# Kernel tuning notes

Measured on AMD Instinct MI355X. Metric: run time of the kernel, lower is better.

## Reference

```python
import jax, jax.numpy as jnp
import numpy as np

N = 100_000   # number of sparse points
C = 128       # channels
K3 = 27       # 3x3x3 kernel offsets


def sparse_conv(x, nbr, W, b):
    """Minkowski-style sparse conv: gather-GEMM-scatter.
    x:   [N, Cin] point features
    nbr: [N, K3] neighbor index per kernel offset; index N -> missing (zero row)
    W:   [K3, Cin, Cout], b: [Cout]
    """
    x_pad = jnp.concatenate([x, jnp.zeros((1, x.shape[1]), x.dtype)], axis=0)

    def step(acc, wk_nk):
        Wk, nk = wk_nk                      # Wk: [Cin,Cout], nk: [N]
        return acc + x_pad[nk] @ Wk, None   # gather + GEMM, accumulate

    acc0 = jnp.broadcast_to(b, (x.shape[0], W.shape[2])).astype(x.dtype)
    acc, _ = jax.lax.scan(step, acc0, (W, nbr.T))
    return acc


def setup_inputs() -> dict:
    key = jax.random.key(0)
    ks = jax.random.split(key, 12)
    Ch = C // 2

    def w(k, shape, fan_in):
        return jax.random.normal(k, shape, dtype=jnp.float32) / np.sqrt(fan_in)

    x = jax.random.normal(ks[0], (N, C), dtype=jnp.float32)
    # neighbor map; value N means "no neighbor" (maps to zero-padded row)
    nbr = jax.random.randint(ks[1], (N, K3), 0, N + 1, dtype=jnp.int32)

    return {
        "x": x,
        "nbr": nbr,
        "W00": w(ks[2], (K3, C, Ch), K3 * C),   # conv0_0: kxkxk, C -> C/2
        "b00": jnp.zeros((Ch,), jnp.float32),
        "W01": w(ks[3], (K3, Ch, Ch), K3 * Ch),  # conv0_1: kxkxk, C/2 -> C/2
        "b01": jnp.zeros((Ch,), jnp.float32),
        "W10": w(ks[4], (C, Ch), C),             # conv1_0: 1x1x1, C -> C/2
        "b10": jnp.zeros((Ch,), jnp.float32),
        "W11": w(ks[5], (K3, Ch, Ch), K3 * Ch),  # conv1_1: kxkxk, C/2 -> C/2
        "b11": jnp.zeros((Ch,), jnp.float32),
        "W12": w(ks[6], (Ch, Ch), Ch),           # conv1_2: 1x1x1, C/2 -> C/2
        "b12": jnp.zeros((Ch,), jnp.float32),
    }


def reference(x, nbr, W00, b00, W01, b01, W10, b10, W11, b11, W12, b12):
    # branch 0: conv -> relu -> conv
    h0 = jax.nn.relu(sparse_conv(x, nbr, W00, b00))
    out0 = sparse_conv(h0, nbr, W01, b01)
    # branch 1: 1x1 conv -> relu -> conv -> relu -> 1x1 conv
    h1 = jax.nn.relu(x @ W10 + b10)
    h1 = jax.nn.relu(sparse_conv(h1, nbr, W11, b11))
    out1 = h1 @ W12 + b12
    # concat channels, residual add
    return jnp.concatenate([out0, out1], axis=1) + x
```

## Files before the change

### kernel.cpp

```cpp
#include <hip/hip_runtime.h>
#include <hip/hip_bf16.h>
#include <stdint.h>

typedef __bf16 bf16x8 __attribute__((ext_vector_type(8)));
typedef float  f32x4  __attribute__((ext_vector_type(4)));

#define MFMA(A, B, C) __builtin_amdgcn_mfma_f32_16x16x32_bf16((A), (B), (C), 0, 0, 0)

#define LDS_BARRIER() asm volatile("s_waitcnt lgkmcnt(0)\n\ts_barrier" ::: "memory")

static __device__ __forceinline__ unsigned short f2b(float f) {
    union { float f; unsigned int u; } v; v.f = f;
    return (unsigned short)((v.u + 0x7FFFu + ((v.u >> 16) & 1u)) >> 16);
}

__global__ __launch_bounds__(256) void convert_kernel(
    const float* __restrict__ x, unsigned short* __restrict__ xb,
    unsigned short* __restrict__ hb, int N) {
    long long i = (long long)blockIdx.x * blockDim.x + threadIdx.x;
    long long base = i * 4;
    long long nx = (long long)N * 128;
    long long total = nx + 128;
    if (base >= total) return;
    if (base < nx) {
        float4 v = *(const float4*)(x + base);
        ushort4 o;
        o.x = f2b(v.x); o.y = f2b(v.y); o.z = f2b(v.z); o.w = f2b(v.w);
        *(ushort4*)(xb + base) = o;
    } else {
        ushort4 z = make_ushort4(0, 0, 0, 0);
        *(ushort4*)(xb + base) = z;
        *(ushort4*)(hb + base) = z;
    }
}

__global__ __launch_bounds__(256) void pack_kernel(
    const float* __restrict__ W00, const float* __restrict__ W01,
    const float* __restrict__ W10, const float* __restrict__ W11,
    const float* __restrict__ W12,
    unsigned short* __restrict__ wp00, unsigned short* __restrict__ wpC,
    unsigned short* __restrict__ wp10, unsigned short* __restrict__ wp12) {
    int g = blockIdx.x * blockDim.x + threadIdx.x;
    const float* W; int cinSteps; int which;
    if (g < 27648)      { W = W00; cinSteps = 4; which = 0; }
    else if (g < 41472) { g -= 27648; W = W01; cinSteps = 2; which = 1; }
    else if (g < 55296) { g -= 41472; W = W11; cinSteps = 2; which = 2; }
    else if (g < 56320) { g -= 55296; W = W10; cinSteps = 4; which = 3; }
    else if (g < 56832) { g -= 56320; W = W12; cinSteps = 2; which = 4; }
    else return;
    int lane = g & 63;
    int st   = g >> 6;
    int t    = st & 3;
    int s    = st >> 2;
    int q = lane >> 4, n16 = lane & 15;
    int k    = s / cinSteps;
    int cinb = (s % cinSteps) * 32;
    int Cin  = cinSteps * 32;
    int cout = t * 16 + n16;
    unsigned short o[8];
#pragma unroll
    for (int j = 0; j < 8; ++j) {
        float v = W[(size_t)(k * Cin + cinb + q * 8 + j) * 64 + cout];
        o[j] = f2b(v);
    }
    unsigned short* dst;
    if (which == 0)      dst = wp00 + (size_t)g * 8;
    else if (which == 1) dst = wpC + (size_t)k * 8192 +
                               ((size_t)(((s & 1) * 4 + t) * 64 + lane)) * 8;
    else if (which == 2) dst = wpC + (size_t)k * 8192 + 4096 +
                               ((size_t)(((s & 1) * 4 + t) * 64 + lane)) * 8;
    else if (which == 3) dst = wp10 + (size_t)g * 8;
    else                 dst = wp12 + (size_t)g * 8;
    *(ushort4*)(dst)     = make_ushort4(o[0], o[1], o[2], o[3]);
    *(ushort4*)(dst + 4) = make_ushort4(o[4], o[5], o[6], o[7]);
}

__global__ __launch_bounds__(256, 2) void passB_kernel(
    const unsigned short* __restrict__ xb, const int* __restrict__ nbr,
    const unsigned short* __restrict__ wp00, const unsigned short* __restrict__ wp10,
    const float* __restrict__ b00, const float* __restrict__ b10,
    unsigned short* __restrict__ hb, int N) {
    __shared__ __align__(16) unsigned short bbuf[2][8192];
    __shared__ __align__(16) int lds_idx[256 * 27];
    const int tid  = threadIdx.x;
    const int lane = tid & 63;
    const int wv   = tid >> 6;
    const int q = lane >> 4, n16 = lane & 15;
    const int rowbase = blockIdx.x * 256 + wv * 64;

    int4 br[4];
#pragma unroll
    for (int j = 0; j < 4; ++j) br[j] = *(const int4*)(wp00 + j * 2048 + tid * 8);
    {
        long long gbase = (long long)blockIdx.x * 256 * 27;
        long long lim = (long long)N * 27 - 1;
        for (int i = tid; i < 6912; i += 256) {
            long long gi = gbase + i; if (gi > lim) gi = lim;
            lds_idx[i] = nbr[gi];
        }
    }
#pragma unroll
    for (int j = 0; j < 4; ++j) *(int4*)(&bbuf[0][j * 2048 + tid * 8]) = br[j];
    __syncthreads();

    f32x4 acc0[4][4];
    f32x4 acc1[4][4];
#pragma unroll
    for (int rs = 0; rs < 4; ++rs)
#pragma unroll
        for (int t = 0; t < 4; ++t) { acc0[rs][t] = (f32x4)0.f; acc1[rs][t] = (f32x4)0.f; }

    int idxb[4], own[4];
#pragma unroll
    for (int rs = 0; rs < 4; ++rs) {
        idxb[rs] = (wv * 64 + rs * 16 + n16) * 27;
        own[rs]  = min(rowbase + rs * 16 + n16, N - 1);
    }

    bf16x8 D[4][4];
#pragma unroll
    for (int rs = 0; rs < 4; ++rs) {
        const unsigned short* p = xb + (size_t)lds_idx[idxb[rs]] * 128 + q * 8;
#pragma unroll
        for (int s2 = 0; s2 < 4; ++s2) D[rs][s2] = *(const bf16x8*)(p + s2 * 32);
    }

    for (int k = 0; k < 27; ++k) {
        int buf = k & 1;
        if (k < 26) {
            const unsigned short* src = wp00 + (size_t)(k + 1) * 8192;
#pragma unroll
            for (int j = 0; j < 4; ++j) br[j] = *(const int4*)(src + j * 2048 + tid * 8);
        }
        bf16x8 Dn[4][4];
#pragma unroll
        for (int rs = 0; rs < 4; ++rs) {
            int ian = (k + 1 < 27) ? lds_idx[idxb[rs] + k + 1] : own[rs];
            const unsigned short* p = xb + (size_t)ian * 128 + q * 8;
#pragma unroll
            for (int s2 = 0; s2 < 4; ++s2) Dn[rs][s2] = *(const bf16x8*)(p + s2 * 32);
        }
        const unsigned short* lb = &bbuf[buf][0];
#pragma unroll
        for (int s2 = 0; s2 < 4; ++s2) {
#pragma unroll
            for (int t = 0; t < 4; ++t) {
                bf16x8 B = *(const bf16x8*)(lb + (s2 * 4 + t) * 512 + lane * 8);
#pragma unroll
                for (int rs = 0; rs < 4; ++rs)
                    acc0[rs][t] = MFMA(D[rs][s2], B, acc0[rs][t]);
            }
        }
        if (k < 26) {
#pragma unroll
            for (int j = 0; j < 4; ++j)
                *(int4*)(&bbuf[buf ^ 1][j * 2048 + tid * 8]) = br[j];
        }
#pragma unroll
        for (int rs = 0; rs < 4; ++rs)
#pragma unroll
            for (int s2 = 0; s2 < 4; ++s2) D[rs][s2] = Dn[rs][s2];
        LDS_BARRIER();
    }

#pragma unroll
    for (int s2 = 0; s2 < 4; ++s2) {
#pragma unroll
        for (int t = 0; t < 4; ++t) {
            bf16x8 B = *(const bf16x8*)(wp10 + s2 * 2048 + t * 512 + lane * 8);
#pragma unroll
            for (int rs = 0; rs < 4; ++rs)
                acc1[rs][t] = MFMA(D[rs][s2], B, acc1[rs][t]);
        }
    }

#pragma unroll
    for (int rs = 0; rs < 4; ++rs)
#pragma unroll
        for (int t = 0; t < 4; ++t) {
            int col = t * 16 + n16;
            float bb0 = b00[col], bb1 = b10[col];
#pragma unroll
            for (int r = 0; r < 4; ++r) {
                int row = rowbase + rs * 16 + q * 4 + r;
                if (row < N) {
                    hb[(size_t)row * 128 + col]      = f2b(fmaxf(acc0[rs][t][r] + bb0, 0.f));
                    hb[(size_t)row * 128 + 64 + col] = f2b(fmaxf(acc1[rs][t][r] + bb1, 0.f));
                }
            }
        }
}

__global__ __launch_bounds__(256, 3) void passC_kernel(
    const unsigned short* __restrict__ hb, const int* __restrict__ nbr,
    const float* __restrict__ x,
    const unsigned short* __restrict__ wpC, const unsigned short* __restrict__ wp12,
    const float* __restrict__ b01, const float* __restrict__ b11,
    const float* __restrict__ b12, float* __restrict__ out, int N) {
    __shared__ __align__(16) unsigned short bbuf[2][4096];
    __shared__ __align__(16) int lds_idx[128 * 27];
    const int tid  = threadIdx.x;
    const int lane = tid & 63;
    const int wv   = tid >> 6;
    const int q = lane >> 4, n16 = lane & 15;
    const int rowbase = blockIdx.x * 128 + wv * 32;

    int idxb[2];
#pragma unroll
    for (int rs = 0; rs < 2; ++rs) idxb[rs] = (wv * 32 + rs * 16 + n16) * 27;

    {
        int4 br[2];
#pragma unroll
        for (int j = 0; j < 2; ++j) br[j] = *(const int4*)(wpC + j * 2048 + tid * 8);
        {
            long long gbase = (long long)blockIdx.x * 128 * 27;
            long long lim = (long long)N * 27 - 1;
            for (int i = tid; i < 3456; i += 256) {
                long long gi = gbase + i; if (gi > lim) gi = lim;
                lds_idx[i] = nbr[gi];
            }
        }
#pragma unroll
        for (int j = 0; j < 2; ++j) *(int4*)(&bbuf[0][j * 2048 + tid * 8]) = br[j];
        __syncthreads();

        f32x4 accA[2][4];
#pragma unroll
        for (int rs = 0; rs < 2; ++rs)
#pragma unroll
            for (int t = 0; t < 4; ++t) accA[rs][t] = (f32x4)0.f;

        bf16x8 Da[2][2], Db[2][2], Dc[2][2];
#pragma unroll
        for (int rs = 0; rs < 2; ++rs) {
            const unsigned short* p0 = hb + (size_t)lds_idx[idxb[rs] + 0] * 128 + q * 8;
            Da[rs][0] = *(const bf16x8*)(p0);
            Da[rs][1] = *(const bf16x8*)(p0 + 32);
            const unsigned short* p1 = hb + (size_t)lds_idx[idxb[rs] + 1] * 128 + q * 8;
            Db[rs][0] = *(const bf16x8*)(p1);
            Db[rs][1] = *(const bf16x8*)(p1 + 32);
        }

        for (int k = 0; k < 27; ++k) {
            int buf = k & 1;
            if (k < 26) {
                const unsigned short* src = wpC + (size_t)(k + 1) * 8192;
#pragma unroll
                for (int j = 0; j < 2; ++j)
                    br[j] = *(const int4*)(src + j * 2048 + tid * 8);
            }
#pragma unroll
            for (int rs = 0; rs < 2; ++rs) {
                int j2 = min(k + 2, 26);
                const unsigned short* p =
                    hb + (size_t)lds_idx[idxb[rs] + j2] * 128 + q * 8;
                Dc[rs][0] = *(const bf16x8*)(p);
                Dc[rs][1] = *(const bf16x8*)(p + 32);
            }
            const unsigned short* lb = &bbuf[buf][0];
#pragma unroll
            for (int s2 = 0; s2 < 2; ++s2) {
#pragma unroll
                for (int t = 0; t < 4; ++t) {
                    bf16x8 B = *(const bf16x8*)(lb + (s2 * 4 + t) * 512 + lane * 8);
#pragma unroll
                    for (int rs = 0; rs < 2; ++rs)
                        accA[rs][t] = MFMA(Da[rs][s2], B, accA[rs][t]);
                }
            }
            if (k < 26) {
#pragma unroll
                for (int j = 0; j < 2; ++j)
                    *(int4*)(&bbuf[buf ^ 1][j * 2048 + tid * 8]) = br[j];
            }
#pragma unroll
            for (int rs = 0; rs < 2; ++rs)
#pragma unroll
                for (int s2 = 0; s2 < 2; ++s2) {
                    Da[rs][s2] = Db[rs][s2]; Db[rs][s2] = Dc[rs][s2];
                }
            LDS_BARRIER();
        }

#pragma unroll
        for (int rs = 0; rs < 2; ++rs)
#pragma unroll
            for (int t = 0; t < 4; ++t) {
                int col = t * 16 + n16;
                float bo = b01[col];
#pragma unroll
                for (int r = 0; r < 4; ++r) {
                    int row = rowbase + rs * 16 + q * 4 + r;
                    if (row < N) {
                        float xv = __builtin_nontemporal_load(x + (size_t)row * 128 + col);
                        __builtin_nontemporal_store(accA[rs][t][r] + bo + xv,
                                                    out + (size_t)row * 128 + col);
                    }
                }
            }
    }

    {
        int4 br[2];
#pragma unroll
        for (int j = 0; j < 2; ++j)
            br[j] = *(const int4*)(wpC + 4096 + j * 2048 + tid * 8);
#pragma unroll
        for (int j = 0; j < 2; ++j) *(int4*)(&bbuf[0][j * 2048 + tid * 8]) = br[j];
        __syncthreads();

        f32x4 accT[2][4];
#pragma unroll
        for (int rs = 0; rs < 2; ++rs)
#pragma unroll
            for (int t = 0; t < 4; ++t) accT[rs][t] = (f32x4)0.f;

        bf16x8 Da[2][2], Db[2][2], Dc[2][2];
#pragma unroll
        for (int rs = 0; rs < 2; ++rs) {
            const unsigned short* p0 =
                hb + (size_t)lds_idx[idxb[rs] + 0] * 128 + 64 + q * 8;
            Da[rs][0] = *(const bf16x8*)(p0);
            Da[rs][1] = *(const bf16x8*)(p0 + 32);
            const unsigned short* p1 =
                hb + (size_t)lds_idx[idxb[rs] + 1] * 128 + 64 + q * 8;
            Db[rs][0] = *(const bf16x8*)(p1);
            Db[rs][1] = *(const bf16x8*)(p1 + 32);
        }

        for (int k = 0; k < 27; ++k) {
            int buf = k & 1;
            if (k < 26) {
                const unsigned short* src = wpC + 4096 + (size_t)(k + 1) * 8192;
#pragma unroll
                for (int j = 0; j < 2; ++j)
                    br[j] = *(const int4*)(src + j * 2048 + tid * 8);
            }
#pragma unroll
            for (int rs = 0; rs < 2; ++rs) {
                int j2 = min(k + 2, 26);
                const unsigned short* p =
                    hb + (size_t)lds_idx[idxb[rs] + j2] * 128 + 64 + q * 8;
                Dc[rs][0] = *(const bf16x8*)(p);
                Dc[rs][1] = *(const bf16x8*)(p + 32);
            }
            const unsigned short* lb = &bbuf[buf][0];
#pragma unroll
            for (int s2 = 0; s2 < 2; ++s2) {
#pragma unroll
                for (int t = 0; t < 4; ++t) {
                    bf16x8 B = *(const bf16x8*)(lb + (s2 * 4 + t) * 512 + lane * 8);
#pragma unroll
                    for (int rs = 0; rs < 2; ++rs)
                        accT[rs][t] = MFMA(Da[rs][s2], B, accT[rs][t]);
                }
            }
            if (k < 26) {
#pragma unroll
                for (int j = 0; j < 2; ++j)
                    *(int4*)(&bbuf[buf ^ 1][j * 2048 + tid * 8]) = br[j];
            }
#pragma unroll
            for (int rs = 0; rs < 2; ++rs)
#pragma unroll
                for (int s2 = 0; s2 < 2; ++s2) {
                    Da[rs][s2] = Db[rs][s2]; Db[rs][s2] = Dc[rs][s2];
                }
            LDS_BARRIER();
        }

        unsigned short* myl = (wv < 3) ? ((unsigned short*)lds_idx + wv * 2304)
                                       : &bbuf[0][0];
#pragma unroll
        for (int rs = 0; rs < 2; ++rs)
#pragma unroll
            for (int t = 0; t < 4; ++t) {
                int col = t * 16 + n16;
                float bt = b11[col];
#pragma unroll
                for (int r = 0; r < 4; ++r) {
                    float tv = fmaxf(accT[rs][t][r] + bt, 0.f);
                    myl[(rs * 16 + q * 4 + r) * 72 + col] = f2b(tv);
                }
            }

        f32x4 accO1[2][4];
#pragma unroll
        for (int rs = 0; rs < 2; ++rs)
#pragma unroll
            for (int t = 0; t < 4; ++t) accO1[rs][t] = (f32x4)0.f;
#pragma unroll
        for (int s2 = 0; s2 < 2; ++s2) {
#pragma unroll
            for (int t = 0; t < 4; ++t) {
                bf16x8 B = *(const bf16x8*)(wp12 + s2 * 2048 + t * 512 + lane * 8);
#pragma unroll
                for (int rs = 0; rs < 2; ++rs) {
                    bf16x8 A = *(const bf16x8*)(myl + (rs * 16 + n16) * 72 + s2 * 32 + q * 8);
                    accO1[rs][t] = MFMA(A, B, accO1[rs][t]);
                }
            }
        }
#pragma unroll
        for (int rs = 0; rs < 2; ++rs)
#pragma unroll
            for (int t = 0; t < 4; ++t) {
                int col = t * 16 + n16;
                float bo = b12[col];
#pragma unroll
                for (int r = 0; r < 4; ++r) {
                    int row = rowbase + rs * 16 + q * 4 + r;
                    if (row < N) {
                        float xv = __builtin_nontemporal_load(x + (size_t)row * 128 + 64 + col);
                        __builtin_nontemporal_store(accO1[rs][t][r] + bo + xv,
                                                    out + (size_t)row * 128 + 64 + col);
                    }
                }
            }
    }
}

extern "C" void kernel_launch(void* const* d_in, const int* in_sizes, int n_in,
                              void* d_out, int out_size, void* d_ws, size_t ws_size,
                              hipStream_t stream) {
    const float* x   = (const float*)d_in[0];
    const int*   nbr = (const int*)d_in[1];
    const float* W00 = (const float*)d_in[2];
    const float* b00 = (const float*)d_in[3];
    const float* W01 = (const float*)d_in[4];
    const float* b01 = (const float*)d_in[5];
    const float* W10 = (const float*)d_in[6];
    const float* b10 = (const float*)d_in[7];
    const float* W11 = (const float*)d_in[8];
    const float* b11 = (const float*)d_in[9];
    const float* W12 = (const float*)d_in[10];
    const float* b12 = (const float*)d_in[11];
    float* out = (float*)d_out;
    int N = in_sizes[0] / 128;

    char* ws = (char*)d_ws;
    size_t cur = 0;
    unsigned short* xb  = (unsigned short*)(ws + cur); cur += (size_t)(N + 1) * 128 * 2;
    unsigned short* hb  = (unsigned short*)(ws + cur); cur += (size_t)(N + 1) * 128 * 2;
    unsigned short* wp00 = (unsigned short*)(ws + cur); cur += 27648 * 8 * 2;
    unsigned short* wpC  = (unsigned short*)(ws + cur); cur += (size_t)27 * 8192 * 2;
    unsigned short* wp10 = (unsigned short*)(ws + cur); cur += 8192 * 2;
    unsigned short* wp12 = (unsigned short*)(ws + cur); cur += 4096 * 2;

    long long cvt_groups = ((long long)N * 128 + 128) / 4;
    int cvt_blocks = (int)((cvt_groups + 255) / 256);
    convert_kernel<<<cvt_blocks, 256, 0, stream>>>(x, xb, hb, N);
    pack_kernel<<<222, 256, 0, stream>>>(W00, W01, W10, W11, W12,
                                         wp00, wpC, wp10, wp12);
    int nstripsB = (N + 255) / 256;
    passB_kernel<<<nstripsB, 256, 0, stream>>>(xb, nbr, wp00, wp10, b00, b10, hb, N);
    int nstripsC = (N + 127) / 128;
    passC_kernel<<<nstripsC, 256, 0, stream>>>(hb, nbr, x, wpC, wp12,
                                               b01, b11, b12, out, N);
}
```

Baseline: 393.1 us.

## Split passB input channels into two phases and merge prep kernels

The first sparse conv is restructured into two passes over the 128 input channels, 64 at a time. Each pass gathers only half of every neighbor row and stages half the weight tile, which halves the LDS weight buffer and the register footprint of the gathered fragments, aiming for better occupancy and latency hiding. In exchange, each neighbor row is gathered twice at half width and the 27-step loop with its barriers runs twice. The convert and pack kernels are also merged into one launch to save a kernel launch.

```diff
diff --git a/kernel.cpp b/kernel.cpp
--- a/kernel.cpp
+++ b/kernel.cpp
@@ -14,33 +14,33 @@
     return (unsigned short)((v.u + 0x7FFFu + ((v.u >> 16) & 1u)) >> 16);
 }
 
-__global__ __launch_bounds__(256) void convert_kernel(
+__global__ __launch_bounds__(256) void prep_kernel(
     const float* __restrict__ x, unsigned short* __restrict__ xb,
-    unsigned short* __restrict__ hb, int N) {
-    long long i = (long long)blockIdx.x * blockDim.x + threadIdx.x;
-    long long base = i * 4;
-    long long nx = (long long)N * 128;
-    long long total = nx + 128;
-    if (base >= total) return;
-    if (base < nx) {
-        float4 v = *(const float4*)(x + base);
-        ushort4 o;
-        o.x = f2b(v.x); o.y = f2b(v.y); o.z = f2b(v.z); o.w = f2b(v.w);
-        *(ushort4*)(xb + base) = o;
-    } else {
-        ushort4 z = make_ushort4(0, 0, 0, 0);
-        *(ushort4*)(xb + base) = z;
-        *(ushort4*)(hb + base) = z;
-    }
-}
-
-__global__ __launch_bounds__(256) void pack_kernel(
+    unsigned short* __restrict__ hb, int N, int cvtBlocks,
     const float* __restrict__ W00, const float* __restrict__ W01,
     const float* __restrict__ W10, const float* __restrict__ W11,
     const float* __restrict__ W12,
     unsigned short* __restrict__ wp00, unsigned short* __restrict__ wpC,
     unsigned short* __restrict__ wp10, unsigned short* __restrict__ wp12) {
-    int g = blockIdx.x * blockDim.x + threadIdx.x;
+    if (blockIdx.x < (unsigned)cvtBlocks) {
+        long long i = (long long)blockIdx.x * blockDim.x + threadIdx.x;
+        long long base = i * 4;
+        long long nx = (long long)N * 128;
+        long long total = nx + 128;
+        if (base >= total) return;
+        if (base < nx) {
+            float4 v = *(const float4*)(x + base);
+            ushort4 o;
+            o.x = f2b(v.x); o.y = f2b(v.y); o.z = f2b(v.z); o.w = f2b(v.w);
+            *(ushort4*)(xb + base) = o;
+        } else {
+            ushort4 z = make_ushort4(0, 0, 0, 0);
+            *(ushort4*)(xb + base) = z;
+            *(ushort4*)(hb + base) = z;
+        }
+        return;
+    }
+    int g = (blockIdx.x - cvtBlocks) * blockDim.x + threadIdx.x;
     const float* W; int cinSteps; int which;
     if (g < 27648)      { W = W00; cinSteps = 4; which = 0; }
     else if (g < 41472) { g -= 27648; W = W01; cinSteps = 2; which = 1; }
@@ -80,7 +80,7 @@
     const unsigned short* __restrict__ wp00, const unsigned short* __restrict__ wp10,
     const float* __restrict__ b00, const float* __restrict__ b10,
     unsigned short* __restrict__ hb, int N) {
-    __shared__ __align__(16) unsigned short bbuf[2][8192];
+    __shared__ __align__(16) unsigned short bbuf[2][4096];
     __shared__ __align__(16) int lds_idx[256 * 27];
     const int tid  = threadIdx.x;
     const int lane = tid & 63;
@@ -88,21 +88,6 @@
     const int q = lane >> 4, n16 = lane & 15;
     const int rowbase = blockIdx.x * 256 + wv * 64;
 
-    int4 br[4];
-#pragma unroll
-    for (int j = 0; j < 4; ++j) br[j] = *(const int4*)(wp00 + j * 2048 + tid * 8);
-    {
-        long long gbase = (long long)blockIdx.x * 256 * 27;
-        long long lim = (long long)N * 27 - 1;
-        for (int i = tid; i < 6912; i += 256) {
-            long long gi = gbase + i; if (gi > lim) gi = lim;
-            lds_idx[i] = nbr[gi];
-        }
-    }
-#pragma unroll
-    for (int j = 0; j < 4; ++j) *(int4*)(&bbuf[0][j * 2048 + tid * 8]) = br[j];
-    __syncthreads();
-
     f32x4 acc0[4][4];
     f32x4 acc1[4][4];
 #pragma unroll
@@ -117,60 +102,81 @@
         own[rs]  = min(rowbase + rs * 16 + n16, N - 1);
     }
 
-    bf16x8 D[4][4];
-#pragma unroll
-    for (int rs = 0; rs < 4; ++rs) {
-        const unsigned short* p = xb + (size_t)lds_idx[idxb[rs]] * 128 + q * 8;
-#pragma unroll
-        for (int s2 = 0; s2 < 4; ++s2) D[rs][s2] = *(const bf16x8*)(p + s2 * 32);
-    }
-
-    for (int k = 0; k < 27; ++k) {
-        int buf = k & 1;
-        if (k < 26) {
-            const unsigned short* src = wp00 + (size_t)(k + 1) * 8192;
-#pragma unroll
-            for (int j = 0; j < 4; ++j) br[j] = *(const int4*)(src + j * 2048 + tid * 8);
-        }
-        bf16x8 Dn[4][4];
+#pragma unroll
+    for (int ph = 0; ph < 2; ++ph) {
+        const int choff = ph * 64;
+        int4 br[2];
+#pragma unroll
+        for (int j = 0; j < 2; ++j)
+            br[j] = *(const int4*)(wp00 + ph * 4096 + j * 2048 + tid * 8);
+        if (ph == 0) {
+            long long gbase = (long long)blockIdx.x * 256 * 27;
+            long long lim = (long long)N * 27 - 1;
+            for (int i = tid; i < 6912; i += 256) {
+                long long gi = gbase + i; if (gi > lim) gi = lim;
+                lds_idx[i] = nbr[gi];
+            }
+        }
+#pragma unroll
+        for (int j = 0; j < 2; ++j) *(int4*)(&bbuf[0][j * 2048 + tid * 8]) = br[j];
+        __syncthreads();
+
+        bf16x8 D[4][2], Dn[4][2];
 #pragma unroll
         for (int rs = 0; rs < 4; ++rs) {
-            int ian = (k + 1 < 27) ? lds_idx[idxb[rs] + k + 1] : own[rs];
-            const unsigned short* p = xb + (size_t)ian * 128 + q * 8;
-#pragma unroll
-            for (int s2 = 0; s2 < 4; ++s2) Dn[rs][s2] = *(const bf16x8*)(p + s2 * 32);
-        }
-        const unsigned short* lb = &bbuf[buf][0];
-#pragma unroll
-        for (int s2 = 0; s2 < 4; ++s2) {
+            const unsigned short* p =
+                xb + (size_t)lds_idx[idxb[rs]] * 128 + choff + q * 8;
+            D[rs][0] = *(const bf16x8*)(p);
+            D[rs][1] = *(const bf16x8*)(p + 32);
+        }
+
+        for (int k = 0; k < 27; ++k) {
+            int buf = k & 1;
+            if (k < 26) {
+                const unsigned short* src = wp00 + ph * 4096 + (size_t)(k + 1) * 8192;
+#pragma unroll
+                for (int j = 0; j < 2; ++j)
+                    br[j] = *(const int4*)(src + j * 2048 + tid * 8);
+            }
+#pragma unroll
+            for (int rs = 0; rs < 4; ++rs) {
+                int ian = (k + 1 < 27) ? lds_idx[idxb[rs] + k + 1] : own[rs];
+                const unsigned short* p = xb + (size_t)ian * 128 + choff + q * 8;
+                Dn[rs][0] = *(const bf16x8*)(p);
+                Dn[rs][1] = *(const bf16x8*)(p + 32);
+            }
+            const unsigned short* lb = &bbuf[buf][0];
+#pragma unroll
+            for (int s2 = 0; s2 < 2; ++s2) {
+#pragma unroll
+                for (int t = 0; t < 4; ++t) {
+                    bf16x8 B = *(const bf16x8*)(lb + (s2 * 4 + t) * 512 + lane * 8);
+#pragma unroll
+                    for (int rs = 0; rs < 4; ++rs)
+                        acc0[rs][t] = MFMA(D[rs][s2], B, acc0[rs][t]);
+                }
+            }
+            if (k < 26) {
+#pragma unroll
+                for (int j = 0; j < 2; ++j)
+                    *(int4*)(&bbuf[buf ^ 1][j * 2048 + tid * 8]) = br[j];
+            }
+#pragma unroll
+            for (int rs = 0; rs < 4; ++rs)
+#pragma unroll
+                for (int s2 = 0; s2 < 2; ++s2) D[rs][s2] = Dn[rs][s2];
+            LDS_BARRIER();
+        }
+
+#pragma unroll
+        for (int s2 = 0; s2 < 2; ++s2) {
 #pragma unroll
             for (int t = 0; t < 4; ++t) {
-                bf16x8 B = *(const bf16x8*)(lb + (s2 * 4 + t) * 512 + lane * 8);
+                bf16x8 B = *(const bf16x8*)(wp10 + ((ph * 2 + s2) * 4 + t) * 512 + lane * 8);
 #pragma unroll
                 for (int rs = 0; rs < 4; ++rs)
-                    acc0[rs][t] = MFMA(D[rs][s2], B, acc0[rs][t]);
-            }
-        }
-        if (k < 26) {
-#pragma unroll
-            for (int j = 0; j < 4; ++j)
-                *(int4*)(&bbuf[buf ^ 1][j * 2048 + tid * 8]) = br[j];
-        }
-#pragma unroll
-        for (int rs = 0; rs < 4; ++rs)
-#pragma unroll
-            for (int s2 = 0; s2 < 4; ++s2) D[rs][s2] = Dn[rs][s2];
-        LDS_BARRIER();
-    }
-
-#pragma unroll
-    for (int s2 = 0; s2 < 4; ++s2) {
-#pragma unroll
-        for (int t = 0; t < 4; ++t) {
-            bf16x8 B = *(const bf16x8*)(wp10 + s2 * 2048 + t * 512 + lane * 8);
-#pragma unroll
-            for (int rs = 0; rs < 4; ++rs)
-                acc1[rs][t] = MFMA(D[rs][s2], B, acc1[rs][t]);
+                    acc1[rs][t] = MFMA(D[rs][s2], B, acc1[rs][t]);
+            }
         }
     }
 
@@ -450,9 +456,9 @@
 
     long long cvt_groups = ((long long)N * 128 + 128) / 4;
     int cvt_blocks = (int)((cvt_groups + 255) / 256);
-    convert_kernel<<<cvt_blocks, 256, 0, stream>>>(x, xb, hb, N);
-    pack_kernel<<<222, 256, 0, stream>>>(W00, W01, W10, W11, W12,
-                                         wp00, wpC, wp10, wp12);
+    prep_kernel<<<cvt_blocks + 222, 256, 0, stream>>>(
+        x, xb, hb, N, cvt_blocks,
+        W00, W01, W10, W11, W12, wp00, wpC, wp10, wp12);
     int nstripsB = (N + 255) / 256;
     passB_kernel<<<nstripsB, 256, 0, stream>>>(xb, nbr, wp00, wp10, b00, b10, hb, N);
     int nstripsC = (N + 127) / 128;
```

After: 390.2 us. No clear change (-0.7%).
